# Kernel optimization log

Hardware: AMD Instinct MI355X
Metric: run time of the kernel (lower is better)

## Reference

```python
import jax, jax.numpy as jnp
import numpy as np

EPS = 1e-5  # config.layer_norm_epsilon

def setup_inputs() -> dict:
    key = jax.random.key(0)
    ks = jax.random.split(key, 3)
    B, S, NX, A, H, O = 16, 2048, 1024, 20, 50, 3
    x = jax.random.normal(ks[0], (B, S, NX), dtype=jnp.float32)
    ln_g = jnp.ones((A, NX), jnp.float32)
    ln_b = jnp.zeros((A, NX), jnp.float32)
    W1 = jax.random.normal(ks[1], (A, NX, H), dtype=jnp.float32) * (1.0 / np.sqrt(NX))
    b1 = jnp.zeros((A, H), jnp.float32)
    W2 = jax.random.normal(ks[2], (A, H, O), dtype=jnp.float32) * (1.0 / np.sqrt(H))
    b2 = jnp.zeros((A, O), jnp.float32)
    return {"x": x, "ln_g": ln_g, "ln_b": ln_b, "W1": W1, "b1": b1, "W2": W2, "b2": b2}

def reference(x, ln_g, ln_b, W1, b1, W2, b2):
    B, S, NX = x.shape
    A = ln_g.shape[0]
    # shared normalization (per-token mean/var), per-adapter affine folded into W1
    mu = jnp.mean(x, axis=-1, keepdims=True)
    var = jnp.mean(jnp.square(x - mu), axis=-1, keepdims=True)  # biased, like torch LN
    xn = (x - mu) * jax.lax.rsqrt(var + EPS)                    # [B,S,NX]
    W1g = ln_g[:, :, None] * W1                                 # [A,NX,H], absorbs LN gamma
    off = jnp.einsum('an,anh->ah', ln_b, W1) + b1               # [A,H],   absorbs LN beta
    h = jax.nn.relu(jnp.einsum('bsn,anh->bash', xn, W1g) + off[None, :, None, :])  # [B,A,S,H]
    o = jnp.einsum('bash,aho->baso', h, W2) + b2[None, :, None, :]                 # [B,A,S,3]
    out = o.reshape(B, A, S * o.shape[-1])                      # [B,A,S*3] (row-major == torch view)
    # squash over the adapter/capsule axis (dim=-1 of [B,S*3,A] == axis 1 here)
    sq = jnp.sum(jnp.square(out), axis=1, keepdims=True)
    scale = sq / (1.0 + sq)
    return scale * out * jax.lax.rsqrt(sq)
```

## Files before the change

kernel.cpp:

```cpp
#include <hip/hip_runtime.h>
#include <hip/hip_bf16.h>
#include <stdint.h>


typedef _Float16 h8 __attribute__((ext_vector_type(8)));
typedef float f4 __attribute__((ext_vector_type(4)));
typedef __attribute__((address_space(1))) void gvoid;
typedef __attribute__((address_space(3))) void lvoid;

__device__ __forceinline__ void cp16(const void* g, void* l) {
  __builtin_amdgcn_global_load_lds((gvoid*)g, (lvoid*)l, 16, 0, 0);
}

__global__ __launch_bounds__(256) void ln_kernel(const float* __restrict__ x,
                                                 _Float16* __restrict__ xn) {
  const int t = threadIdx.x, w = t >> 6, l = t & 63;
  const int tok = blockIdx.x * 4 + w;
  const float4* xr = (const float4*)(x + (size_t)tok * 1024);
  float4 v0 = xr[l * 2], v1 = xr[l * 2 + 1];
  float4 v2 = xr[128 + l * 2], v3 = xr[128 + l * 2 + 1];
  float s1 = (v0.x + v0.y + v0.z + v0.w) + (v1.x + v1.y + v1.z + v1.w) +
             (v2.x + v2.y + v2.z + v2.w) + (v3.x + v3.y + v3.z + v3.w);
  float s2 = v0.x * v0.x + v0.y * v0.y + v0.z * v0.z + v0.w * v0.w;
  s2 += v1.x * v1.x + v1.y * v1.y + v1.z * v1.z + v1.w * v1.w;
  s2 += v2.x * v2.x + v2.y * v2.y + v2.z * v2.z + v2.w * v2.w;
  s2 += v3.x * v3.x + v3.y * v3.y + v3.z * v3.z + v3.w * v3.w;
#pragma unroll
  for (int m = 32; m > 0; m >>= 1) {
    s1 += __shfl_xor(s1, m);
    s2 += __shfl_xor(s2, m);
  }
  const float mu = s1 * 0.0009765625f;
  const float var = s2 * 0.0009765625f - mu * mu;
  const float inv = rsqrtf(var + 1e-5f);
  union { _Float16 h[8]; uint4 u; } p;
  _Float16* xw = xn + (size_t)tok * 1024 + l * 8;
  p.h[0] = (_Float16)((v0.x - mu) * inv); p.h[1] = (_Float16)((v0.y - mu) * inv);
  p.h[2] = (_Float16)((v0.z - mu) * inv); p.h[3] = (_Float16)((v0.w - mu) * inv);
  p.h[4] = (_Float16)((v1.x - mu) * inv); p.h[5] = (_Float16)((v1.y - mu) * inv);
  p.h[6] = (_Float16)((v1.z - mu) * inv); p.h[7] = (_Float16)((v1.w - mu) * inv);
  *(uint4*)xw = p.u;
  p.h[0] = (_Float16)((v2.x - mu) * inv); p.h[1] = (_Float16)((v2.y - mu) * inv);
  p.h[2] = (_Float16)((v2.z - mu) * inv); p.h[3] = (_Float16)((v2.w - mu) * inv);
  p.h[4] = (_Float16)((v3.x - mu) * inv); p.h[5] = (_Float16)((v3.y - mu) * inv);
  p.h[6] = (_Float16)((v3.z - mu) * inv); p.h[7] = (_Float16)((v3.w - mu) * inv);
  *(uint4*)(xw + 512) = p.u;
}

__global__ __launch_bounds__(256) void prep_w(const float* __restrict__ ln_g,
                                              const float* __restrict__ ln_b,
                                              const float* __restrict__ W1,
                                              _Float16* __restrict__ wB,
                                              float* __restrict__ offacc) {
  const int a = blockIdx.x, k0 = blockIdx.y * 64, t = threadIdx.x;
  __shared__ float tw[3200];
  __shared__ float gg[64], bb[64];
  const float* src = W1 + (size_t)(a * 1024 + k0) * 50;
  for (int i = t; i < 3200; i += 256) tw[i] = src[i];
  if (t < 64) gg[t] = ln_g[a * 1024 + k0 + t];
  else if (t < 128) bb[t - 64] = ln_b[a * 1024 + k0 + (t - 64)];
  __syncthreads();
  const int h = t & 63, q = t >> 6;
  if (h < 50) {
    float po = 0.f;
#pragma unroll
    for (int half = 0; half < 2; ++half) {
      union { _Float16 hh[8]; uint4 u; } pk;
#pragma unroll
      for (int j = 0; j < 8; ++j) {
        const int k = q * 16 + half * 8 + j;
        const float wv = tw[k * 50 + h];
        pk.hh[j] = (_Float16)(gg[k] * wv);
        po += bb[k] * wv;
      }
      *(uint4*)(wB + (size_t)(a * 50 + h) * 1024 + k0 + q * 16 + half * 8) =
          pk.u;
    }
    if (po != 0.f) atomicAdd(&offacc[a * 50 + h], po);
  }
  if (a == 0 && t < 192) {
    const uint4 z = {0, 0, 0, 0};
    *(uint4*)(wB + (size_t)(1000 + (t >> 3)) * 1024 + k0 + (t & 7) * 8) = z;
  }
}

__global__ __launch_bounds__(256, 4) void gemm_kernel(
    const _Float16* __restrict__ xn, const _Float16* __restrict__ wB,
    const float* __restrict__ offacc, const float* __restrict__ b1,
    const float* __restrict__ W2, float* __restrict__ out) {
  __shared__ __align__(16) char smem[36448];
  const int g = blockIdx.x;
  const int xcd = g & 7, i0 = g >> 3;
  const int nb = i0 & 7;
  const int mb = xcd * 32 + (i0 >> 3);
  const int t = threadIdx.x, w = t >> 6, l = t & 63;

  const int a0 = (nb * 128) / 50;
  float* w2s = (float*)(smem + 34048);
  for (int i = t; i < 600; i += 256) {
    const int j = i / 150, a = a0 + j;
    w2s[i] = (a < 20) ? W2[a * 150 + (i - j * 150)] : 0.f;
  }

  const int lr = l >> 3;
  const int ksl = (l & 7) ^ lr;
  const _Float16* gA = xn + (size_t)(mb * 128 + lr) * 1024 + ksl * 8;
  const _Float16* gB = wB + (size_t)(nb * 128 + lr) * 1024 + ksl * 8;

  const int rowA = ((w >> 1) * 64) + (l & 15);
  const int rowB = ((w & 1) * 64) + (l & 15);
  const int kq = l >> 4;
  const int xa = rowA & 7, xb = rowB & 7;
  const char* pA = smem + rowA * 128;
  const char* pB = smem + 16384 + rowB * 128;

  f4 acc[4][4];
  {
    f4 z = {0.f, 0.f, 0.f, 0.f};
#pragma unroll
    for (int mt = 0; mt < 4; ++mt)
#pragma unroll
      for (int nt = 0; nt < 4; ++nt) acc[mt][nt] = z;
  }

  for (int kt = 0; kt < 16; ++kt) {
#pragma unroll
    for (int i = 0; i < 4; ++i) {
      const int chunk = w * 4 + i;
      cp16(gA + (size_t)chunk * 8192 + kt * 64, smem + chunk * 1024);
      cp16(gB + (size_t)chunk * 8192 + kt * 64, smem + 16384 + chunk * 1024);
    }
    __syncthreads();
#pragma unroll
    for (int ks = 0; ks < 2; ++ks) {
      h8 af[4], bf[4];
      const int sl = ks * 4 + kq;
#pragma unroll
      for (int mt = 0; mt < 4; ++mt)
        af[mt] = *(const h8*)(pA + mt * 2048 + ((sl ^ xa) << 4));
#pragma unroll
      for (int nt = 0; nt < 4; ++nt)
        bf[nt] = *(const h8*)(pB + nt * 2048 + ((sl ^ xb) << 4));
#pragma unroll
      for (int mt = 0; mt < 4; ++mt)
#pragma unroll
        for (int nt = 0; nt < 4; ++nt)
          acc[mt][nt] = __builtin_amdgcn_mfma_f32_16x16x32_f16(
              af[mt], bf[nt], acc[mt][nt], 0, 0, 0);
    }
    __syncthreads();
  }

  float offt[4];
#pragma unroll
  for (int nt = 0; nt < 4; ++nt) {
    const int n = nb * 128 + rowB + nt * 16;
    offt[nt] = offacc[n] + ((n < 1000) ? b1[n] : 0.f);
  }

  const int ml = t >> 2, j = t & 3;
  const int a = a0 + j;
  const int c0 = nb * 128;
  int cs = a * 50, ce = cs + 50;
  if (cs < c0) cs = c0;
  if (ce > c0 + 128) ce = c0 + 128;
  const bool act = (a < 20) && (cs < ce);
  const int lo = cs - c0;
  const int len = act ? (ce - cs) : 0;
  const int h0 = cs - a * 50;
  const float* wrow = w2s + j * 150 + h0 * 3;

  float* hm = (float*)smem;
  const int mrl = (l >> 4) * 4;
  const int ncol = (w & 1) * 64 + (l & 15);
#pragma unroll
  for (int p = 0; p < 2; ++p) {
    if (p) __syncthreads();
    if ((w >> 1) == p) {
#pragma unroll
      for (int mt = 0; mt < 4; ++mt)
#pragma unroll
        for (int nt = 0; nt < 4; ++nt)
#pragma unroll
          for (int r = 0; r < 4; ++r)
            hm[(mrl + mt * 16 + r) * 133 + (ncol + nt * 16)] =
                fmaxf(acc[mt][nt][r] + offt[nt], 0.f);
    }
    __syncthreads();
    if (act) {
      const float* hr = hm + ml * 133 + lo;
      float o0 = 0.f, o1 = 0.f, o2 = 0.f;
      for (int i = 0; i < len; ++i) {
        const float hv = hr[i];
        o0 += hv * wrow[i * 3 + 0];
        o1 += hv * wrow[i * 3 + 1];
        o2 += hv * wrow[i * 3 + 2];
      }
      const int tok = mb * 128 + p * 64 + ml;
      const int b = tok >> 11, s = tok & 2047;
      float* op = out + ((size_t)(b * 20 + a) * 2048 + (size_t)s) * 3;
      atomicAdd(op + 0, o0);
      atomicAdd(op + 1, o1);
      atomicAdd(op + 2, o2);
    }
  }
}

__global__ __launch_bounds__(256) void squash_kernel(
    float* __restrict__ out, const float* __restrict__ b2) {
  const int idx = blockIdx.x * 256 + threadIdx.x;
  const int b = idx / 6144;
  const int rem = idx - b * 6144;
  const int oi = rem % 3;
  float v[20];
  float sq = 0.f;
#pragma unroll
  for (int a = 0; a < 20; ++a) {
    v[a] = out[((size_t)(b * 20 + a)) * 6144 + rem] + b2[a * 3 + oi];
    sq += v[a] * v[a];
  }
  const float f = sqrtf(sq) / (1.f + sq);
#pragma unroll
  for (int a = 0; a < 20; ++a)
    out[((size_t)(b * 20 + a)) * 6144 + rem] = v[a] * f;
}

extern "C" void kernel_launch(void* const* d_in, const int* in_sizes, int n_in,
                              void* d_out, int out_size, void* d_ws,
                              size_t ws_size, hipStream_t stream) {
  const float* x    = (const float*)d_in[0];
  const float* ln_g = (const float*)d_in[1];
  const float* ln_b = (const float*)d_in[2];
  const float* W1   = (const float*)d_in[3];
  const float* b1   = (const float*)d_in[4];
  const float* W2   = (const float*)d_in[5];
  const float* b2   = (const float*)d_in[6];
  float* out = (float*)d_out;

  char* ws = (char*)d_ws;
  float* offacc = (float*)ws;
  _Float16* wBw = (_Float16*)(ws + 4096);
  _Float16* xnw = (_Float16*)(ws + 4096 + 2097152);

  hipMemsetAsync(offacc, 0, 1024 * sizeof(float), stream);
  hipMemsetAsync(out, 0, (size_t)out_size * sizeof(float), stream);
  prep_w<<<dim3(20, 16), 256, 0, stream>>>(ln_g, ln_b, W1, wBw, offacc);
  ln_kernel<<<8192, 256, 0, stream>>>(x, xnw);
  gemm_kernel<<<2048, 256, 0, stream>>>(xnw, wBw, offacc, b1, W2, out);
  squash_kernel<<<384, 256, 0, stream>>>(out, b2);
}
```

Before: 311.1 us.

## Replace memsets and atomics with partial offsets, selective zeroing and direct stores

Drops the two memsets. Adapters whose 50-column range straddles a 128-column tile boundary (2,5,7,10,12,15,17) are zeroed by extra blocks in prep_w, and adapters fully inside a tile now get plain stores instead of atomics. The LN-beta offset is now written as 16 per-k-chunk partial sums that gemm_kernel adds itself, replacing float atomics. ln_kernel load/store indexing is also changed to contiguous per-lane float4 loads with 8-byte half stores. The output is correct only if the zeroing blocks in prep_w finish before gemm's atomics, which same-stream ordering ensures. The cost is 16 extra loads per column in the gemm epilogue.

```diff
diff --git a/kernel.cpp b/kernel.cpp
--- a/kernel.cpp
+++ b/kernel.cpp
@@ -17,8 +17,7 @@
   const int t = threadIdx.x, w = t >> 6, l = t & 63;
   const int tok = blockIdx.x * 4 + w;
   const float4* xr = (const float4*)(x + (size_t)tok * 1024);
-  float4 v0 = xr[l * 2], v1 = xr[l * 2 + 1];
-  float4 v2 = xr[128 + l * 2], v3 = xr[128 + l * 2 + 1];
+  float4 v0 = xr[l], v1 = xr[64 + l], v2 = xr[128 + l], v3 = xr[192 + l];
   float s1 = (v0.x + v0.y + v0.z + v0.w) + (v1.x + v1.y + v1.z + v1.w) +
              (v2.x + v2.y + v2.z + v2.w) + (v3.x + v3.y + v3.z + v3.w);
   float s2 = v0.x * v0.x + v0.y * v0.y + v0.z * v0.z + v0.w * v0.w;
@@ -33,36 +32,48 @@
   const float mu = s1 * 0.0009765625f;
   const float var = s2 * 0.0009765625f - mu * mu;
   const float inv = rsqrtf(var + 1e-5f);
-  union { _Float16 h[8]; uint4 u; } p;
-  _Float16* xw = xn + (size_t)tok * 1024 + l * 8;
-  p.h[0] = (_Float16)((v0.x - mu) * inv); p.h[1] = (_Float16)((v0.y - mu) * inv);
-  p.h[2] = (_Float16)((v0.z - mu) * inv); p.h[3] = (_Float16)((v0.w - mu) * inv);
-  p.h[4] = (_Float16)((v1.x - mu) * inv); p.h[5] = (_Float16)((v1.y - mu) * inv);
-  p.h[6] = (_Float16)((v1.z - mu) * inv); p.h[7] = (_Float16)((v1.w - mu) * inv);
-  *(uint4*)xw = p.u;
-  p.h[0] = (_Float16)((v2.x - mu) * inv); p.h[1] = (_Float16)((v2.y - mu) * inv);
-  p.h[2] = (_Float16)((v2.z - mu) * inv); p.h[3] = (_Float16)((v2.w - mu) * inv);
-  p.h[4] = (_Float16)((v3.x - mu) * inv); p.h[5] = (_Float16)((v3.y - mu) * inv);
-  p.h[6] = (_Float16)((v3.z - mu) * inv); p.h[7] = (_Float16)((v3.w - mu) * inv);
-  *(uint4*)(xw + 512) = p.u;
+  uint2* xw = (uint2*)(xn + (size_t)tok * 1024);
+  union { _Float16 h[4]; uint2 u; } q;
+#define CVT_STORE(V, OFF)                                   \
+  q.h[0] = (_Float16)((V.x - mu) * inv);                    \
+  q.h[1] = (_Float16)((V.y - mu) * inv);                    \
+  q.h[2] = (_Float16)((V.z - mu) * inv);                    \
+  q.h[3] = (_Float16)((V.w - mu) * inv);                    \
+  xw[(OFF) + l] = q.u;
+  CVT_STORE(v0, 0)
+  CVT_STORE(v1, 64)
+  CVT_STORE(v2, 128)
+  CVT_STORE(v3, 192)
+#undef CVT_STORE
 }
 
 __global__ __launch_bounds__(256) void prep_w(const float* __restrict__ ln_g,
                                               const float* __restrict__ ln_b,
                                               const float* __restrict__ W1,
                                               _Float16* __restrict__ wB,
-                                              float* __restrict__ offacc) {
-  const int a = blockIdx.x, k0 = blockIdx.y * 64, t = threadIdx.x;
+                                              float* __restrict__ offpart,
+                                              float* __restrict__ out) {
+  const int t = threadIdx.x;
+  if (blockIdx.x >= 320) {
+    static const int sa[7] = {2, 5, 7, 10, 12, 15, 17};
+    const int idx = blockIdx.x - 320;
+    const int ai = idx >> 4, bi = idx & 15;
+    float4* dst = (float4*)(out + ((size_t)(bi * 20 + sa[ai])) * 6144);
+    const float4 z4 = {0.f, 0.f, 0.f, 0.f};
+    for (int i = t; i < 1536; i += 256) dst[i] = z4;
+    return;
+  }
+  const int a = blockIdx.x >> 4, k0 = (blockIdx.x & 15) * 64;
   __shared__ float tw[3200];
-  __shared__ float gg[64], bb[64];
+  __shared__ float gg[64], bb[64], red[256];
   const float* src = W1 + (size_t)(a * 1024 + k0) * 50;
   for (int i = t; i < 3200; i += 256) tw[i] = src[i];
   if (t < 64) gg[t] = ln_g[a * 1024 + k0 + t];
   else if (t < 128) bb[t - 64] = ln_b[a * 1024 + k0 + (t - 64)];
   __syncthreads();
   const int h = t & 63, q = t >> 6;
+  float po = 0.f;
   if (h < 50) {
-    float po = 0.f;
 #pragma unroll
     for (int half = 0; half < 2; ++half) {
       union { _Float16 hh[8]; uint4 u; } pk;
@@ -76,8 +87,12 @@
       *(uint4*)(wB + (size_t)(a * 50 + h) * 1024 + k0 + q * 16 + half * 8) =
           pk.u;
     }
-    if (po != 0.f) atomicAdd(&offacc[a * 50 + h], po);
-  }
+  }
+  red[t] = po;
+  __syncthreads();
+  if (t < 50)
+    offpart[(blockIdx.x & 15) * 1024 + a * 50 + t] =
+        red[t] + red[64 + t] + red[128 + t] + red[192 + t];
   if (a == 0 && t < 192) {
     const uint4 z = {0, 0, 0, 0};
     *(uint4*)(wB + (size_t)(1000 + (t >> 3)) * 1024 + k0 + (t & 7) * 8) = z;
@@ -86,7 +101,7 @@
 
 __global__ __launch_bounds__(256, 4) void gemm_kernel(
     const _Float16* __restrict__ xn, const _Float16* __restrict__ wB,
-    const float* __restrict__ offacc, const float* __restrict__ b1,
+    const float* __restrict__ offpart, const float* __restrict__ b1,
     const float* __restrict__ W2, float* __restrict__ out) {
   __shared__ __align__(16) char smem[36448];
   const int g = blockIdx.x;
@@ -152,11 +167,16 @@
   }
 
   float offt[4];
+  int ncols[4];
 #pragma unroll
   for (int nt = 0; nt < 4; ++nt) {
-    const int n = nb * 128 + rowB + nt * 16;
-    offt[nt] = offacc[n] + ((n < 1000) ? b1[n] : 0.f);
-  }
+    ncols[nt] = nb * 128 + rowB + nt * 16;
+    offt[nt] = (ncols[nt] < 1000) ? b1[ncols[nt]] : 0.f;
+  }
+#pragma unroll
+  for (int c = 0; c < 16; ++c)
+#pragma unroll
+    for (int nt = 0; nt < 4; ++nt) offt[nt] += offpart[c * 1024 + ncols[nt]];
 
   const int ml = t >> 2, j = t & 3;
   const int a = a0 + j;
@@ -199,9 +219,13 @@
       const int tok = mb * 128 + p * 64 + ml;
       const int b = tok >> 11, s = tok & 2047;
       float* op = out + ((size_t)(b * 20 + a) * 2048 + (size_t)s) * 3;
-      atomicAdd(op + 0, o0);
-      atomicAdd(op + 1, o1);
-      atomicAdd(op + 2, o2);
+      if (len == 50) {
+        op[0] = o0; op[1] = o1; op[2] = o2;
+      } else {
+        atomicAdd(op + 0, o0);
+        atomicAdd(op + 1, o1);
+        atomicAdd(op + 2, o2);
+      }
     }
   }
 }
@@ -238,14 +262,12 @@
   float* out = (float*)d_out;
 
   char* ws = (char*)d_ws;
-  float* offacc = (float*)ws;
-  _Float16* wBw = (_Float16*)(ws + 4096);
-  _Float16* xnw = (_Float16*)(ws + 4096 + 2097152);
-
-  hipMemsetAsync(offacc, 0, 1024 * sizeof(float), stream);
-  hipMemsetAsync(out, 0, (size_t)out_size * sizeof(float), stream);
-  prep_w<<<dim3(20, 16), 256, 0, stream>>>(ln_g, ln_b, W1, wBw, offacc);
+  float* offpart = (float*)ws;
+  _Float16* wBw  = (_Float16*)(ws + 65536);
+  _Float16* xnw  = (_Float16*)(ws + 65536 + 2097152);
+
+  prep_w<<<432, 256, 0, stream>>>(ln_g, ln_b, W1, wBw, offpart, out);
   ln_kernel<<<8192, 256, 0, stream>>>(x, xnw);
-  gemm_kernel<<<2048, 256, 0, stream>>>(xnw, wBw, offacc, b1, W2, out);
+  gemm_kernel<<<2048, 256, 0, stream>>>(xnw, wBw, offpart, b1, W2, out);
   squash_kernel<<<384, 256, 0, stream>>>(out, b2);
 }
```

Measured after the change: 303.9 us. 1.02x faster.
